# Kernel tuning notes

Hardware: AMD Instinct MI355X
Metric: run time of the kernel (lower is better)

## Reference

```python
import jax, jax.numpy as jnp
import numpy as np

B, T, K = 32, 8192, 16
EPS = 1e-7
LAM_FIRE, LAM_CANCEL, LAM_VALID, LAM_WRITE = 1.0, 1.0, 0.5, 0.5


def setup_inputs() -> dict:
    key = jax.random.key(0)
    ks = jax.random.split(key, 11)
    return {
        "trigger_hazard": jax.random.uniform(ks[0], (B, T, K), jnp.float32),
        "validity": jax.random.uniform(ks[1], (B, T, K), jnp.float32),
        "cancel_logits": jax.random.normal(ks[2], (B, T, K, 3), jnp.float32),
        "write_score": jax.random.normal(ks[3], (B, T, 1), jnp.float32),
        "live_mask": jax.random.randint(ks[4], (B, T, K), 0, 2).astype(bool),
        "contract_id": jax.random.randint(ks[5], (B, T, K), 0, 32),
        "oracle_fire": jax.random.randint(ks[6], (B, T, K), 0, 2).astype(jnp.float32),
        "oracle_cancel": jax.random.randint(ks[7], (B, T, K), 0, 4),
        "oracle_valid": jax.random.randint(ks[8], (B, T, K), 0, 2).astype(jnp.float32),
        "oracle_should_write": jax.random.randint(ks[9], (B, T, 1), 0, 2).astype(jnp.float32),
        "oracle_contract_id": jax.random.randint(ks[10], (B, T, K), 0, 32),
    }


def _masked_bce(p_raw, y, m):
    # Mirrors torch: BCE(clamp(p)*mask, y*mask), then *mask, sum / clamp(mask.sum(),1)
    n = jnp.maximum(m.sum(), 1.0)
    p = jnp.clip(p_raw, EPS, 1.0 - EPS) * m
    t = y * m
    # extra inner clip only guards masked entries (p==0), which are zeroed anyway
    bce = -(t * jnp.log(jnp.clip(p, EPS)) + (1.0 - t) * jnp.log(jnp.clip(1.0 - p, EPS)))
    return (bce * m).sum() / n


def _cancel_ce(logits, cancel_tgt, live_mask):
    has = ((cancel_tgt > 0) & live_mask).astype(jnp.float32)  # (B,T,K)
    n = has.sum()
    tgt = jnp.clip(cancel_tgt - 1, 0).astype(jnp.int32)
    logp = jax.nn.log_softmax(logits, axis=-1)  # (B,T,K,3)
    ce = -jnp.take_along_axis(logp, tgt[..., None], axis=-1)[..., 0]
    return jnp.where(n > 0, (ce * has).sum() / jnp.maximum(n, 1.0), 0.0)


def _bce_with_logits(x, y):
    return jnp.mean(jnp.maximum(x, 0.0) - x * y + jnp.log1p(jnp.exp(-jnp.abs(x))))


def reference(trigger_hazard, validity, cancel_logits, write_score, live_mask,
              contract_id, oracle_fire, oracle_cancel, oracle_valid,
              oracle_should_write, oracle_contract_id):
    # Vectorized align_oracle_to_model: broadcast compare + first-match argmax + gather
    match = (contract_id[..., :, None] == oracle_contract_id[..., None, :]) \
            & (contract_id != 0)[..., None]              # (B,T,Km,Ko)
    found = match.any(axis=-1)                           # (B,T,Km)
    idx = jnp.argmax(match, axis=-1)                     # first matching oracle slot

    def align_f(x):  # float tensors -> zeros where unmatched (torch out = zeros float)
        return jnp.where(found, jnp.take_along_axis(x, idx, axis=2), 0.0)

    fire_t = align_f(oracle_fire)
    valid_t = align_f(oracle_valid)
    cancel_t = jnp.where(found, jnp.take_along_axis(oracle_cancel, idx, axis=2), 0)

    m = live_mask.astype(jnp.float32)
    fire = LAM_FIRE * _masked_bce(trigger_hazard, fire_t, m)
    cancel = LAM_CANCEL * _cancel_ce(cancel_logits, cancel_t, live_mask)
    valid = LAM_VALID * _masked_bce(validity, valid_t, m)
    write = LAM_WRITE * _bce_with_logits(write_score, oracle_should_write)
    total = fire + cancel + valid + write
    return jnp.stack([fire, cancel, valid, write, total])
```

## Files before the change

kernel.cpp:

```cpp
#include <hip/hip_runtime.h>
#include <math.h>

#define EPS_F 1e-7f

constexpr int Bc = 32, Tc = 8192, Kc = 16;
constexpr int ROWS   = Bc * Tc;
constexpr int BLOCK  = 256;
constexpr int NITEM4 = ROWS * 4;
constexpr int NTILE  = NITEM4 / BLOCK;
constexpr int NBLK   = 512;
constexpr int TPB    = NTILE / NBLK;

constexpr int W_OCID = 0;
constexpr int W_OCAN = 1024;
constexpr int W_OFIR = 2048;
constexpr int W_OVAL = 3072;
constexpr int W_CID  = 4096;
constexpr int W_LIVE = 5120;
constexpr int W_TRIG = 6144;
constexpr int W_VALP = 7168;
constexpr int W_CLOG = 8192;
constexpr int W_WSC  = 11264;
constexpr int W_OSW  = 11520;
constexpr int BUFB   = 11776;
constexpr int DEPTH  = 2;
constexpr int SMEM_BYTES = 4 * DEPTH * BUFB;

typedef unsigned long long u64;

__device__ __forceinline__ u64 shflx64(u64 v, int m) {
  unsigned lo = __shfl_xor((unsigned)v, m, 64);
  unsigned hi = __shfl_xor((unsigned)(v >> 32), m, 64);
  return ((u64)hi << 32) | lo;
}

__device__ __forceinline__ void dma16(void* lds, const void* g) {
  __builtin_amdgcn_global_load_lds(
      (const __attribute__((address_space(1))) void*)g,
      (__attribute__((address_space(3))) void*)lds, 16, 0, 0);
}
__device__ __forceinline__ void dma4(void* lds, const void* g) {
  __builtin_amdgcn_global_load_lds(
      (const __attribute__((address_space(1))) void*)g,
      (__attribute__((address_space(3))) void*)lds, 4, 0, 0);
}

#define WAITCNT_VM(N)                                                      \
  do {                                                                     \
    asm volatile("s_waitcnt vmcnt(" #N ")" ::: "memory");                  \
    __builtin_amdgcn_sched_barrier(0);                                     \
  } while (0)

__device__ __forceinline__ void stage_tile(
    char* sb, int gt, int w, int lane,
    const char* trig, const char* valp, const char* clog, const char* wscore,
    const char* live, const char* cid, const char* ofire, const char* ocan,
    const char* ovalid, const char* oshw, const char* ocid)
{
  const size_t o16 = (size_t)(gt * 256 + w * 64 + lane) * 16;
  dma16(sb + W_OCID, ocid   + o16);
  dma16(sb + W_OCAN, ocan   + o16);
  dma16(sb + W_OFIR, ofire  + o16);
  dma16(sb + W_OVAL, ovalid + o16);
  dma16(sb + W_CID,  cid    + o16);
  dma16(sb + W_LIVE, live   + o16);
  dma16(sb + W_TRIG, trig   + o16);
  dma16(sb + W_VALP, valp   + o16);
  const char* gc = clog + (size_t)(gt * 256 + w * 64) * 48;
  dma16(sb + W_CLOG + 0,    gc + 0    + lane * 16);
  dma16(sb + W_CLOG + 1024, gc + 1024 + lane * 16);
  dma16(sb + W_CLOG + 2048, gc + 2048 + lane * 16);
  const size_t ro = (size_t)(gt * 64 + lane) * 4;
  dma4(sb + W_WSC, wscore + ro);
  dma4(sb + W_OSW, oshw   + ro);
}

__global__ __launch_bounds__(BLOCK) void loss_main(
    const float* __restrict__ trig,
    const float* __restrict__ valp,
    const float* __restrict__ clog,
    const float* __restrict__ wscore,
    const int*   __restrict__ live,
    const int*   __restrict__ cid,
    const float* __restrict__ ofire,
    const int*   __restrict__ ocan,
    const float* __restrict__ ovalid,
    const float* __restrict__ oshw,
    const int*   __restrict__ ocid,
    float* __restrict__ part)
{
  __shared__ __align__(16) char smem[SMEM_BYTES];

  const int tid  = threadIdx.x;
  const int lane = tid & 63;
  const int w    = tid >> 6;
  const int gt0  = blockIdx.x * TPB;

  const char* trig_b   = (const char*)trig;
  const char* valp_b   = (const char*)valp;
  const char* clog_b   = (const char*)clog;
  const char* wscore_b = (const char*)wscore;
  const char* live_b   = (const char*)live;
  const char* cid_b    = (const char*)cid;
  const char* ofire_b  = (const char*)ofire;
  const char* ocan_b   = (const char*)ocan;
  const char* ovalid_b = (const char*)ovalid;
  const char* oshw_b   = (const char*)oshw;
  const char* ocid_b   = (const char*)ocid;

  char* wb = smem + (size_t)w * (DEPTH * BUFB);

  stage_tile(wb, gt0, w, lane, trig_b, valp_b, clog_b, wscore_b, live_b,
             cid_b, ofire_b, ocan_b, ovalid_b, oshw_b, ocid_b);

  float a0 = 0.f, a1 = 0.f, a2 = 0.f, a3 = 0.f, a4 = 0.f, a5 = 0.f;

  for (int t = 0; t < TPB; ++t) {
    char* sb = wb + (t & 1) * BUFB;

    if (t + 1 < TPB) {
      asm volatile("s_waitcnt lgkmcnt(0)" ::: "memory");
      stage_tile(wb + ((t + 1) & 1) * BUFB, gt0 + t + 1, w, lane,
                 trig_b, valp_b, clog_b, wscore_b, live_b, cid_b,
                 ofire_b, ocan_b, ovalid_b, oshw_b, ocid_b);
      WAITCNT_VM(13);
    } else {
      WAITCNT_VM(0);
    }

    const int4   oc = *(const int4*)  (sb + W_OCID + lane * 16);
    const int4   cc = *(const int4*)  (sb + W_OCAN + lane * 16);
    const float4 ff = *(const float4*)(sb + W_OFIR + lane * 16);
    const float4 vv = *(const float4*)(sb + W_OVAL + lane * 16);
    const int4   cd = *(const int4*)  (sb + W_CID  + lane * 16);
    const int4   lm = *(const int4*)  (sb + W_LIVE + lane * 16);
    const float4 ph = *(const float4*)(sb + W_TRIG + lane * 16);
    const float4 pq = *(const float4*)(sb + W_VALP + lane * 16);
    const float4 lA = *(const float4*)(sb + W_CLOG + lane * 48 + 0);
    const float4 lB = *(const float4*)(sb + W_CLOG + lane * 48 + 16);
    const float4 lC = *(const float4*)(sb + W_CLOG + lane * 48 + 32);
    const float  wx = *(const float*) (sb + W_WSC + (tid >> 2) * 4);
    const float  wy = *(const float*) (sb + W_OSW + (tid >> 2) * 4);

    u64 tblLo = 0ull, tblHi = 0ull, fndLo = 0ull, fndHi = 0ull;
    {
      const int   ocs[4] = {oc.x, oc.y, oc.z, oc.w};
      const int   ccs[4] = {cc.x, cc.y, cc.z, cc.w};
      const float ffs[4] = {ff.x, ff.y, ff.z, ff.w};
      const float vvs[4] = {vv.x, vv.y, vv.z, vv.w};
      #pragma unroll
      for (int j = 0; j < 4; ++j) {
        const unsigned c  = (unsigned)ocs[j] & 31u;
        const unsigned sh = (c & 15u) * 4u;
        const bool isLo   = c < 16u;
        const bool seen   = (((isLo ? fndLo : fndHi) >> sh) & 1ull) != 0ull;
        const unsigned nib = (unsigned)ffs[j] | ((unsigned)vvs[j] << 1) |
                             ((unsigned)ccs[j] << 2);
        const u64 add  = seen ? 0ull : ((u64)nib << sh);
        const u64 fadd = 0xFull << sh;
        tblLo |= isLo ? add : 0ull;
        tblHi |= isLo ? 0ull : add;
        fndLo |= isLo ? fadd : 0ull;
        fndHi |= isLo ? 0ull : fadd;
      }
    }

    #pragma unroll
    for (int m = 1; m <= 2; m <<= 1) {
      const u64 pTL = shflx64(tblLo, m);
      const u64 pTH = shflx64(tblHi, m);
      const u64 pFL = shflx64(fndLo, m);
      const u64 pFH = shflx64(fndHi, m);
      const bool iLow = (lane & m) == 0;
      const u64 loTL = iLow ? tblLo : pTL, hiTL = iLow ? pTL : tblLo;
      const u64 loTH = iLow ? tblHi : pTH, hiTH = iLow ? pTH : tblHi;
      const u64 loFL = iLow ? fndLo : pFL, hiFL = iLow ? pFL : fndLo;
      const u64 loFH = iLow ? fndHi : pFH, hiFH = iLow ? pFH : fndHi;
      tblLo = loTL | (hiTL & ~loFL);
      tblHi = loTH | (hiTH & ~loFH);
      fndLo = loFL | hiFL;
      fndHi = loFH | hiFH;
    }

    {
      const int   cds[4] = {cd.x, cd.y, cd.z, cd.w};
      const int   lms[4] = {lm.x, lm.y, lm.z, lm.w};
      const float phs[4] = {ph.x, ph.y, ph.z, ph.w};
      const float pqs[4] = {pq.x, pq.y, pq.z, pq.w};
      const float L0[4] = {lA.x, lA.w, lB.z, lC.y};
      const float L1[4] = {lA.y, lB.x, lB.w, lC.z};
      const float L2[4] = {lA.z, lB.y, lC.x, lC.w};
      #pragma unroll
      for (int j = 0; j < 4; ++j) {
        const unsigned c  = (unsigned)cds[j] & 31u;
        const unsigned sh = (c & 15u) * 4u;
        const bool isLo   = c < 16u;
        const bool fnd = (c != 0u) &&
                         ((((isLo ? fndLo : fndHi) >> sh) & 1ull) != 0ull);
        unsigned nib = (unsigned)(((isLo ? tblLo : tblHi) >> sh)) & 15u;
        nib = fnd ? nib : 0u;
        const float fire_t = (float)(nib & 1u);
        const float val_t  = (float)((nib >> 1) & 1u);
        const int   can_t  = (int)(nib >> 2);

        const float m = lms[j] ? 1.f : 0.f;

        const float p  = fminf(fmaxf(phs[j], EPS_F), 1.f - EPS_F);
        const float bf = -__logf((fire_t != 0.f) ? p : 1.f - p);
        const float q  = fminf(fmaxf(pqs[j], EPS_F), 1.f - EPS_F);
        const float bv = -__logf((val_t != 0.f) ? q : 1.f - q);

        const float has = (can_t > 0 && lms[j]) ? 1.f : 0.f;
        const int tgt = (can_t - 1) < 0 ? 0 : (can_t - 1);
        const float l0 = L0[j], l1 = L1[j], l2 = L2[j];
        const float mx  = fmaxf(l0, fmaxf(l1, l2));
        const float lse = mx + __logf(__expf(l0 - mx) + __expf(l1 - mx) +
                                      __expf(l2 - mx));
        const float lt  = (tgt == 0) ? l0 : ((tgt == 1) ? l1 : l2);

        a0 += bf * m;
        a1 += m;
        a2 += (lse - lt) * has;
        a3 += has;
        a4 += bv * m;
      }
    }

    if ((tid & 3) == 0) {
      a5 += fmaxf(wx, 0.f) - wx * wy + __logf(1.f + __expf(-fabsf(wx)));
    }
  }

  float v[6] = {a0, a1, a2, a3, a4, a5};
  #pragma unroll
  for (int off = 32; off > 0; off >>= 1) {
    #pragma unroll
    for (int i = 0; i < 6; ++i) v[i] += __shfl_down(v[i], off, 64);
  }
  __shared__ float red[4][6];
  if (lane == 0) {
    #pragma unroll
    for (int i = 0; i < 6; ++i) red[w][i] = v[i];
  }
  __syncthreads();
  if (tid == 0) {
    #pragma unroll
    for (int i = 0; i < 6; ++i)
      part[blockIdx.x * 6 + i] = red[0][i] + red[1][i] + red[2][i] + red[3][i];
  }
}

__global__ __launch_bounds__(BLOCK) void loss_finalize(
    const float* __restrict__ part, float* __restrict__ out)
{
  double v[6] = {0, 0, 0, 0, 0, 0};
  for (int r = threadIdx.x; r < NBLK; r += BLOCK) {
    #pragma unroll
    for (int i = 0; i < 6; ++i) v[i] += (double)part[r * 6 + i];
  }
  #pragma unroll
  for (int off = 32; off > 0; off >>= 1) {
    #pragma unroll
    for (int i = 0; i < 6; ++i) v[i] += __shfl_down(v[i], off, 64);
  }
  __shared__ double red[4][6];
  const int w = threadIdx.x >> 6, lane = threadIdx.x & 63;
  if (lane == 0) {
    #pragma unroll
    for (int i = 0; i < 6; ++i) red[w][i] = v[i];
  }
  __syncthreads();
  if (threadIdx.x == 0) {
    double a[6];
    #pragma unroll
    for (int i = 0; i < 6; ++i) a[i] = red[0][i] + red[1][i] + red[2][i] + red[3][i];
    const double live_n = a[1] < 1.0 ? 1.0 : a[1];
    const double fire   = a[0] / live_n;
    const double cancel = (a[3] > 0.0) ? a[2] / (a[3] < 1.0 ? 1.0 : a[3])
                                       : 0.0;
    const double valid  = 0.5 * a[4] / live_n;
    const double wr     = 0.5 * a[5] / (double)ROWS;
    out[0] = (float)fire;
    out[1] = (float)cancel;
    out[2] = (float)valid;
    out[3] = (float)wr;
    out[4] = (float)(fire + cancel + valid + wr);
  }
}

extern "C" void kernel_launch(void* const* d_in, const int* in_sizes, int n_in,
                              void* d_out, int out_size, void* d_ws, size_t ws_size,
                              hipStream_t stream) {
  const float* trig   = (const float*)d_in[0];
  const float* valp   = (const float*)d_in[1];
  const float* clog   = (const float*)d_in[2];
  const float* wscore = (const float*)d_in[3];
  const int*   live   = (const int*)  d_in[4];
  const int*   cid    = (const int*)  d_in[5];
  const float* ofire  = (const float*)d_in[6];
  const int*   ocan   = (const int*)  d_in[7];
  const float* ovalid = (const float*)d_in[8];
  const float* oshw   = (const float*)d_in[9];
  const int*   ocid   = (const int*)  d_in[10];
  float* out  = (float*)d_out;
  float* part = (float*)d_ws;

  loss_main<<<NBLK, BLOCK, 0, stream>>>(trig, valp, clog, wscore, live, cid,
                                        ofire, ocan, ovalid, oshw, ocid, part);
  loss_finalize<<<1, BLOCK, 0, stream>>>(part, out);
}
```

Baseline: 215.0 us.

## Replace LDS-staged 4-lane-per-row pipeline with one-thread-per-row direct loads

Removes the double-buffered global_load_lds staging and the 4-lanes-per-row split with its shuffle merge of the lookup tables. Each thread now loads a full row (16 slots plus 48 logits) straight into registers and builds the table by iterating in reverse so the first match wins. The grid grows to one block per 256 rows with a launch bound of 2 blocks per unit. In exchange, each lane's loads are strided by 64 or 192 bytes, which coalesces worse, and register pressure rises sharply with about 100 floats live per thread.

```diff
diff --git a/kernel.cpp b/kernel.cpp
--- a/kernel.cpp
+++ b/kernel.cpp
@@ -4,78 +4,13 @@
 #define EPS_F 1e-7f
 
 constexpr int Bc = 32, Tc = 8192, Kc = 16;
-constexpr int ROWS   = Bc * Tc;
-constexpr int BLOCK  = 256;
-constexpr int NITEM4 = ROWS * 4;
-constexpr int NTILE  = NITEM4 / BLOCK;
-constexpr int NBLK   = 512;
-constexpr int TPB    = NTILE / NBLK;
-
-constexpr int W_OCID = 0;
-constexpr int W_OCAN = 1024;
-constexpr int W_OFIR = 2048;
-constexpr int W_OVAL = 3072;
-constexpr int W_CID  = 4096;
-constexpr int W_LIVE = 5120;
-constexpr int W_TRIG = 6144;
-constexpr int W_VALP = 7168;
-constexpr int W_CLOG = 8192;
-constexpr int W_WSC  = 11264;
-constexpr int W_OSW  = 11520;
-constexpr int BUFB   = 11776;
-constexpr int DEPTH  = 2;
-constexpr int SMEM_BYTES = 4 * DEPTH * BUFB;
+constexpr int ROWS  = Bc * Tc;
+constexpr int BLOCK = 256;
+constexpr int NBLK  = ROWS / BLOCK;
 
 typedef unsigned long long u64;
 
-__device__ __forceinline__ u64 shflx64(u64 v, int m) {
-  unsigned lo = __shfl_xor((unsigned)v, m, 64);
-  unsigned hi = __shfl_xor((unsigned)(v >> 32), m, 64);
-  return ((u64)hi << 32) | lo;
-}
-
-__device__ __forceinline__ void dma16(void* lds, const void* g) {
-  __builtin_amdgcn_global_load_lds(
-      (const __attribute__((address_space(1))) void*)g,
-      (__attribute__((address_space(3))) void*)lds, 16, 0, 0);
-}
-__device__ __forceinline__ void dma4(void* lds, const void* g) {
-  __builtin_amdgcn_global_load_lds(
-      (const __attribute__((address_space(1))) void*)g,
-      (__attribute__((address_space(3))) void*)lds, 4, 0, 0);
-}
-
-#define WAITCNT_VM(N)                                                      \
-  do {                                                                     \
-    asm volatile("s_waitcnt vmcnt(" #N ")" ::: "memory");                  \
-    __builtin_amdgcn_sched_barrier(0);                                     \
-  } while (0)
-
-__device__ __forceinline__ void stage_tile(
-    char* sb, int gt, int w, int lane,
-    const char* trig, const char* valp, const char* clog, const char* wscore,
-    const char* live, const char* cid, const char* ofire, const char* ocan,
-    const char* ovalid, const char* oshw, const char* ocid)
-{
-  const size_t o16 = (size_t)(gt * 256 + w * 64 + lane) * 16;
-  dma16(sb + W_OCID, ocid   + o16);
-  dma16(sb + W_OCAN, ocan   + o16);
-  dma16(sb + W_OFIR, ofire  + o16);
-  dma16(sb + W_OVAL, ovalid + o16);
-  dma16(sb + W_CID,  cid    + o16);
-  dma16(sb + W_LIVE, live   + o16);
-  dma16(sb + W_TRIG, trig   + o16);
-  dma16(sb + W_VALP, valp   + o16);
-  const char* gc = clog + (size_t)(gt * 256 + w * 64) * 48;
-  dma16(sb + W_CLOG + 0,    gc + 0    + lane * 16);
-  dma16(sb + W_CLOG + 1024, gc + 1024 + lane * 16);
-  dma16(sb + W_CLOG + 2048, gc + 2048 + lane * 16);
-  const size_t ro = (size_t)(gt * 64 + lane) * 4;
-  dma4(sb + W_WSC, wscore + ro);
-  dma4(sb + W_OSW, oshw   + ro);
-}
-
-__global__ __launch_bounds__(BLOCK) void loss_main(
+__global__ __launch_bounds__(BLOCK, 2) void loss_main(
     const float* __restrict__ trig,
     const float* __restrict__ valp,
     const float* __restrict__ clog,
@@ -89,147 +24,109 @@
     const int*   __restrict__ ocid,
     float* __restrict__ part)
 {
-  __shared__ __align__(16) char smem[SMEM_BYTES];
-
-  const int tid  = threadIdx.x;
-  const int lane = tid & 63;
-  const int w    = tid >> 6;
-  const int gt0  = blockIdx.x * TPB;
-
-  const char* trig_b   = (const char*)trig;
-  const char* valp_b   = (const char*)valp;
-  const char* clog_b   = (const char*)clog;
-  const char* wscore_b = (const char*)wscore;
-  const char* live_b   = (const char*)live;
-  const char* cid_b    = (const char*)cid;
-  const char* ofire_b  = (const char*)ofire;
-  const char* ocan_b   = (const char*)ocan;
-  const char* ovalid_b = (const char*)ovalid;
-  const char* oshw_b   = (const char*)oshw;
-  const char* ocid_b   = (const char*)ocid;
-
-  char* wb = smem + (size_t)w * (DEPTH * BUFB);
-
-  stage_tile(wb, gt0, w, lane, trig_b, valp_b, clog_b, wscore_b, live_b,
-             cid_b, ofire_b, ocan_b, ovalid_b, oshw_b, ocid_b);
-
-  float a0 = 0.f, a1 = 0.f, a2 = 0.f, a3 = 0.f, a4 = 0.f, a5 = 0.f;
-
-  for (int t = 0; t < TPB; ++t) {
-    char* sb = wb + (t & 1) * BUFB;
-
-    if (t + 1 < TPB) {
-      asm volatile("s_waitcnt lgkmcnt(0)" ::: "memory");
-      stage_tile(wb + ((t + 1) & 1) * BUFB, gt0 + t + 1, w, lane,
-                 trig_b, valp_b, clog_b, wscore_b, live_b, cid_b,
-                 ofire_b, ocan_b, ovalid_b, oshw_b, ocid_b);
-      WAITCNT_VM(13);
-    } else {
-      WAITCNT_VM(0);
+  const int tid = threadIdx.x;
+  const int row = blockIdx.x * BLOCK + tid;
+  const size_t o64  = (size_t)row * 64;
+  const size_t o192 = (size_t)row * 192;
+
+  int4 oc[4]; int4 cc[4]; float4 ff[4]; float4 vv[4];
+  #pragma unroll
+  for (int j = 0; j < 4; ++j) {
+    oc[j] = *(const int4*)  ((const char*)ocid   + o64 + j * 16);
+    cc[j] = *(const int4*)  ((const char*)ocan   + o64 + j * 16);
+    ff[j] = *(const float4*)((const char*)ofire  + o64 + j * 16);
+    vv[j] = *(const float4*)((const char*)ovalid + o64 + j * 16);
+  }
+
+  u64 tblLo = 0ull, tblHi = 0ull, fndLo = 0ull, fndHi = 0ull;
+  #pragma unroll
+  for (int j = 3; j >= 0; --j) {
+    const int   ocs[4] = {oc[j].x, oc[j].y, oc[j].z, oc[j].w};
+    const int   ccs[4] = {cc[j].x, cc[j].y, cc[j].z, cc[j].w};
+    const float ffs[4] = {ff[j].x, ff[j].y, ff[j].z, ff[j].w};
+    const float vvs[4] = {vv[j].x, vv[j].y, vv[j].z, vv[j].w};
+    #pragma unroll
+    for (int s = 3; s >= 0; --s) {
+      const unsigned c   = (unsigned)ocs[s] & 31u;
+      const unsigned sh  = (c & 15u) * 4u;
+      const bool     isLo = c < 16u;
+      const unsigned nib = (unsigned)ffs[s] | ((unsigned)vvs[s] << 1) |
+                           ((unsigned)ccs[s] << 2);
+      const u64 msk = 0xFull << sh;
+      const u64 add = (u64)nib << sh;
+      tblLo = isLo ? ((tblLo & ~msk) | add) : tblLo;
+      tblHi = isLo ? tblHi : ((tblHi & ~msk) | add);
+      fndLo |= isLo ? msk : 0ull;
+      fndHi |= isLo ? 0ull : msk;
     }
-
-    const int4   oc = *(const int4*)  (sb + W_OCID + lane * 16);
-    const int4   cc = *(const int4*)  (sb + W_OCAN + lane * 16);
-    const float4 ff = *(const float4*)(sb + W_OFIR + lane * 16);
-    const float4 vv = *(const float4*)(sb + W_OVAL + lane * 16);
-    const int4   cd = *(const int4*)  (sb + W_CID  + lane * 16);
-    const int4   lm = *(const int4*)  (sb + W_LIVE + lane * 16);
-    const float4 ph = *(const float4*)(sb + W_TRIG + lane * 16);
-    const float4 pq = *(const float4*)(sb + W_VALP + lane * 16);
-    const float4 lA = *(const float4*)(sb + W_CLOG + lane * 48 + 0);
-    const float4 lB = *(const float4*)(sb + W_CLOG + lane * 48 + 16);
-    const float4 lC = *(const float4*)(sb + W_CLOG + lane * 48 + 32);
-    const float  wx = *(const float*) (sb + W_WSC + (tid >> 2) * 4);
-    const float  wy = *(const float*) (sb + W_OSW + (tid >> 2) * 4);
-
-    u64 tblLo = 0ull, tblHi = 0ull, fndLo = 0ull, fndHi = 0ull;
-    {
-      const int   ocs[4] = {oc.x, oc.y, oc.z, oc.w};
-      const int   ccs[4] = {cc.x, cc.y, cc.z, cc.w};
-      const float ffs[4] = {ff.x, ff.y, ff.z, ff.w};
-      const float vvs[4] = {vv.x, vv.y, vv.z, vv.w};
-      #pragma unroll
-      for (int j = 0; j < 4; ++j) {
-        const unsigned c  = (unsigned)ocs[j] & 31u;
-        const unsigned sh = (c & 15u) * 4u;
-        const bool isLo   = c < 16u;
-        const bool seen   = (((isLo ? fndLo : fndHi) >> sh) & 1ull) != 0ull;
-        const unsigned nib = (unsigned)ffs[j] | ((unsigned)vvs[j] << 1) |
-                             ((unsigned)ccs[j] << 2);
-        const u64 add  = seen ? 0ull : ((u64)nib << sh);
-        const u64 fadd = 0xFull << sh;
-        tblLo |= isLo ? add : 0ull;
-        tblHi |= isLo ? 0ull : add;
-        fndLo |= isLo ? fadd : 0ull;
-        fndHi |= isLo ? 0ull : fadd;
-      }
-    }
-
-    #pragma unroll
-    for (int m = 1; m <= 2; m <<= 1) {
-      const u64 pTL = shflx64(tblLo, m);
-      const u64 pTH = shflx64(tblHi, m);
-      const u64 pFL = shflx64(fndLo, m);
-      const u64 pFH = shflx64(fndHi, m);
-      const bool iLow = (lane & m) == 0;
-      const u64 loTL = iLow ? tblLo : pTL, hiTL = iLow ? pTL : tblLo;
-      const u64 loTH = iLow ? tblHi : pTH, hiTH = iLow ? pTH : tblHi;
-      const u64 loFL = iLow ? fndLo : pFL, hiFL = iLow ? pFL : fndLo;
-      const u64 loFH = iLow ? fndHi : pFH, hiFH = iLow ? pFH : fndHi;
-      tblLo = loTL | (hiTL & ~loFL);
-      tblHi = loTH | (hiTH & ~loFH);
-      fndLo = loFL | hiFL;
-      fndHi = loFH | hiFH;
-    }
-
-    {
-      const int   cds[4] = {cd.x, cd.y, cd.z, cd.w};
-      const int   lms[4] = {lm.x, lm.y, lm.z, lm.w};
-      const float phs[4] = {ph.x, ph.y, ph.z, ph.w};
-      const float pqs[4] = {pq.x, pq.y, pq.z, pq.w};
-      const float L0[4] = {lA.x, lA.w, lB.z, lC.y};
-      const float L1[4] = {lA.y, lB.x, lB.w, lC.z};
-      const float L2[4] = {lA.z, lB.y, lC.x, lC.w};
-      #pragma unroll
-      for (int j = 0; j < 4; ++j) {
-        const unsigned c  = (unsigned)cds[j] & 31u;
-        const unsigned sh = (c & 15u) * 4u;
-        const bool isLo   = c < 16u;
-        const bool fnd = (c != 0u) &&
-                         ((((isLo ? fndLo : fndHi) >> sh) & 1ull) != 0ull);
-        unsigned nib = (unsigned)(((isLo ? tblLo : tblHi) >> sh)) & 15u;
-        nib = fnd ? nib : 0u;
-        const float fire_t = (float)(nib & 1u);
-        const float val_t  = (float)((nib >> 1) & 1u);
-        const int   can_t  = (int)(nib >> 2);
-
-        const float m = lms[j] ? 1.f : 0.f;
-
-        const float p  = fminf(fmaxf(phs[j], EPS_F), 1.f - EPS_F);
-        const float bf = -__logf((fire_t != 0.f) ? p : 1.f - p);
-        const float q  = fminf(fmaxf(pqs[j], EPS_F), 1.f - EPS_F);
-        const float bv = -__logf((val_t != 0.f) ? q : 1.f - q);
-
-        const float has = (can_t > 0 && lms[j]) ? 1.f : 0.f;
-        const int tgt = (can_t - 1) < 0 ? 0 : (can_t - 1);
-        const float l0 = L0[j], l1 = L1[j], l2 = L2[j];
-        const float mx  = fmaxf(l0, fmaxf(l1, l2));
-        const float lse = mx + __logf(__expf(l0 - mx) + __expf(l1 - mx) +
-                                      __expf(l2 - mx));
-        const float lt  = (tgt == 0) ? l0 : ((tgt == 1) ? l1 : l2);
-
-        a0 += bf * m;
-        a1 += m;
-        a2 += (lse - lt) * has;
-        a3 += has;
-        a4 += bv * m;
-      }
-    }
-
-    if ((tid & 3) == 0) {
-      a5 += fmaxf(wx, 0.f) - wx * wy + __logf(1.f + __expf(-fabsf(wx)));
-    }
-  }
+  }
+
+  int4 cd[4]; int4 lm[4]; float4 ph[4]; float4 pq[4]; float4 cl[12];
+  #pragma unroll
+  for (int j = 0; j < 4; ++j) {
+    cd[j] = *(const int4*)  ((const char*)cid  + o64 + j * 16);
+    lm[j] = *(const int4*)  ((const char*)live + o64 + j * 16);
+    ph[j] = *(const float4*)((const char*)trig + o64 + j * 16);
+    pq[j] = *(const float4*)((const char*)valp + o64 + j * 16);
+  }
+  #pragma unroll
+  for (int j = 0; j < 12; ++j) {
+    cl[j] = *(const float4*)((const char*)clog + o192 + j * 16);
+  }
+  const float wx = wscore[row];
+  const float wy = oshw[row];
+
+  int   cds[16], lms[16];
+  float phs[16], pqs[16], F[48];
+  #pragma unroll
+  for (int j = 0; j < 4; ++j) {
+    cds[4*j+0]=cd[j].x; cds[4*j+1]=cd[j].y; cds[4*j+2]=cd[j].z; cds[4*j+3]=cd[j].w;
+    lms[4*j+0]=lm[j].x; lms[4*j+1]=lm[j].y; lms[4*j+2]=lm[j].z; lms[4*j+3]=lm[j].w;
+    phs[4*j+0]=ph[j].x; phs[4*j+1]=ph[j].y; phs[4*j+2]=ph[j].z; phs[4*j+3]=ph[j].w;
+    pqs[4*j+0]=pq[j].x; pqs[4*j+1]=pq[j].y; pqs[4*j+2]=pq[j].z; pqs[4*j+3]=pq[j].w;
+  }
+  #pragma unroll
+  for (int j = 0; j < 12; ++j) {
+    F[4*j+0]=cl[j].x; F[4*j+1]=cl[j].y; F[4*j+2]=cl[j].z; F[4*j+3]=cl[j].w;
+  }
+
+  float a0 = 0.f, a1 = 0.f, a2 = 0.f, a3 = 0.f, a4 = 0.f;
+  #pragma unroll
+  for (int k = 0; k < 16; ++k) {
+    const unsigned c  = (unsigned)cds[k] & 31u;
+    const unsigned sh = (c & 15u) * 4u;
+    const bool isLo   = c < 16u;
+    const bool fnd = (c != 0u) &&
+                     ((((isLo ? fndLo : fndHi) >> sh) & 1ull) != 0ull);
+    unsigned nib = (unsigned)(((isLo ? tblLo : tblHi) >> sh)) & 15u;
+    nib = fnd ? nib : 0u;
+    const float fire_t = (float)(nib & 1u);
+    const float val_t  = (float)((nib >> 1) & 1u);
+    const int   can_t  = (int)(nib >> 2);
+
+    const float m = lms[k] ? 1.f : 0.f;
+
+    const float p  = fminf(fmaxf(phs[k], EPS_F), 1.f - EPS_F);
+    const float bf = -__logf((fire_t != 0.f) ? p : 1.f - p);
+    const float q  = fminf(fmaxf(pqs[k], EPS_F), 1.f - EPS_F);
+    const float bv = -__logf((val_t != 0.f) ? q : 1.f - q);
+
+    const float has = (can_t > 0 && lms[k]) ? 1.f : 0.f;
+    const int tgt = (can_t - 1) < 0 ? 0 : (can_t - 1);
+    const float l0 = F[3*k], l1 = F[3*k+1], l2 = F[3*k+2];
+    const float mx  = fmaxf(l0, fmaxf(l1, l2));
+    const float lse = mx + __logf(__expf(l0 - mx) + __expf(l1 - mx) +
+                                  __expf(l2 - mx));
+    const float lt  = (tgt == 0) ? l0 : ((tgt == 1) ? l1 : l2);
+
+    a0 += bf * m;
+    a1 += m;
+    a2 += (lse - lt) * has;
+    a3 += has;
+    a4 += bv * m;
+  }
+
+  const float a5 = fmaxf(wx, 0.f) - wx * wy + __logf(1.f + __expf(-fabsf(wx)));
 
   float v[6] = {a0, a1, a2, a3, a4, a5};
   #pragma unroll
@@ -238,6 +135,7 @@
     for (int i = 0; i < 6; ++i) v[i] += __shfl_down(v[i], off, 64);
   }
   __shared__ float red[4][6];
+  const int lane = tid & 63, w = tid >> 6;
   if (lane == 0) {
     #pragma unroll
     for (int i = 0; i < 6; ++i) red[w][i] = v[i];
```

Result: slower. 231.9 us (+7.9%).
